# Performance work log

Hardware: AMD Instinct MI355X
Metric: run time of the kernel (lower is better)

The kernel has to match this reference:

```python
import jax, jax.numpy as jnp
import numpy as np

BN_EPS = 1e-5
NORM_EPS = 1e-6


def setup_inputs() -> dict:
    key = jax.random.key(0)
    k1, k2, k3, k4 = jax.random.split(key, 4)
    n_total, d = 200000, 128
    n, s = 50000, 25
    features = jax.random.normal(k1, (n_total, d), dtype=jnp.float32)
    self_idx = jax.random.randint(k2, (n,), 0, n_total, dtype=jnp.int64)
    neigh_idx = jax.random.randint(k3, (n, s), 0, n_total, dtype=jnp.int64)
    W = jax.random.normal(k4, (d, 2 * d), dtype=jnp.float32) / jnp.sqrt(2.0 * d)
    b = jnp.zeros((d,), dtype=jnp.float32)
    gamma = jnp.ones((d,), dtype=jnp.float32)
    beta = jnp.zeros((d,), dtype=jnp.float32)
    return {"features": features, "self_idx": self_idx, "neigh_idx": neigh_idx,
            "W": W, "b": b, "gamma": gamma, "beta": beta}


def reference(features, self_idx, neigh_idx, W, b, gamma, beta):
    # mean-aggregate sampled neighbor features: [N, S, D] -> [N, D]
    agg = jnp.mean(features[neigh_idx], axis=1)
    # concat self features with aggregated neighbor features: [N, 2D]
    h = jnp.concatenate([features[self_idx], agg], axis=1)
    # linear -> relu
    out = jax.nn.relu(h @ W.T + b)
    # batchnorm (training mode: batch statistics, biased variance)
    mu = jnp.mean(out, axis=0)
    var = jnp.var(out, axis=0)
    out = (out - mu) * jax.lax.rsqrt(var + BN_EPS) * gamma + beta
    # (dropout p=0 -> identity)
    # row-wise L2 normalize
    norm = jnp.linalg.norm(out, axis=1, keepdims=True)
    return out / (norm + NORM_EPS)
```

## Files before the change

kernel.cpp:

```cpp
#include <hip/hip_runtime.h>
#include <math.h>

typedef __attribute__((ext_vector_type(8))) short short8;
typedef __attribute__((ext_vector_type(4))) float f32x4;
typedef unsigned short ushort_t;
typedef unsigned int uint_t;

#define D 128
#define TWO_D 256
#define S_NEIGH 25

static constexpr float BN_EPS_C = 1e-5f;
static constexpr float NORM_EPS_C = 1e-6f;

__device__ __forceinline__ uint_t f2bf_bits(float f) {
    uint_t u = __float_as_uint(f);
    return (u + 0x7FFFu + ((u >> 16) & 1u)) >> 16;
}

__device__ __forceinline__ void conv8(const float* __restrict__ src, ushort_t* __restrict__ dst) {
    const float4 f0 = *(const float4*)(src);
    const float4 f1 = *(const float4*)(src + 4);
    uint_t o[4];
    o[0] = f2bf_bits(f0.x) | (f2bf_bits(f0.y) << 16);
    o[1] = f2bf_bits(f0.z) | (f2bf_bits(f0.w) << 16);
    o[2] = f2bf_bits(f1.x) | (f2bf_bits(f1.y) << 16);
    o[3] = f2bf_bits(f1.z) | (f2bf_bits(f1.w) << 16);
    *(uint4*)(dst) = *(uint4*)o;
}

__global__ __launch_bounds__(256) void k_conv(const float* __restrict__ feat,
                                              ushort_t* __restrict__ feat16,
                                              const float* __restrict__ W,
                                              ushort_t* __restrict__ Wb,
                                              float* __restrict__ stats) {
    const long i0 = ((long)blockIdx.x * 256 + threadIdx.x) * 8;
    conv8(feat + i0, feat16 + i0);
    if (blockIdx.x < 16) {
        conv8(W + i0, Wb + i0);
    }
    if (blockIdx.x == 16 && threadIdx.x < 256) stats[threadIdx.x] = 0.0f;
}

__global__ __launch_bounds__(256, 3) void k_gather16(
    const ushort_t* __restrict__ feat16,
    const int* __restrict__ self_idx,
    const int* __restrict__ neigh_idx,
    ushort_t* __restrict__ h16, int N)
{
    __shared__ int s_nidx[64 * S_NEIGH];
    __shared__ int s_sidx[64];
    const int t = threadIdx.x;
    const int base = blockIdx.x * 64;
    const int nvalid = min(64, N - base);
    const int V = nvalid * S_NEIGH;
    const long goff = (long)base * S_NEIGH;
    for (int i = t; i < (64 * S_NEIGH) / 4; i += 256) {
        const int e0 = 4 * i;
        if (e0 + 3 < V) {
            ((int4*)s_nidx)[i] = *(const int4*)(neigh_idx + goff + e0);
        } else {
            #pragma unroll
            for (int e = 0; e < 4; ++e)
                if (e0 + e < V) s_nidx[e0 + e] = neigh_idx[goff + e0 + e];
        }
    }
    if (t < 64 && t < nvalid) s_sidx[t] = self_idx[base + t];
    __syncthreads();

    const int g = t >> 4;
    const int l16 = t & 15;
    const int eoff = l16 * 8;
    #pragma unroll
    for (int rep = 0; rep < 4; ++rep) {
        const int n = rep * 16 + g;
        if (n < nvalid) {
            const long gn = base + n;
            const uint4 sf = *(const uint4*)(feat16 + (long)s_sidx[n] * D + eoff);
            *(uint4*)(h16 + gn * TWO_D + eoff) = sf;
            const int* nid = s_nidx + n * S_NEIGH;
            float ae[8] = {0.f,0.f,0.f,0.f,0.f,0.f,0.f,0.f};
            float ao[8] = {0.f,0.f,0.f,0.f,0.f,0.f,0.f,0.f};
            #pragma unroll
            for (int b = 0; b < 2; ++b) {
                uint4 buf[12];
                #pragma unroll
                for (int u = 0; u < 12; ++u)
                    buf[u] = *(const uint4*)(feat16 + (long)nid[b * 12 + u] * D + eoff);
                #pragma unroll
                for (int u = 0; u < 12; ++u) {
                    const uint_t* pu = (const uint_t*)&buf[u];
                    float* ac = (u & 1) ? ao : ae;
                    #pragma unroll
                    for (int j = 0; j < 4; ++j) {
                        const uint_t w = pu[j];
                        ac[2 * j]     += __uint_as_float(w << 16);
                        ac[2 * j + 1] += __uint_as_float(w & 0xFFFF0000u);
                    }
                }
            }
            {
                const uint4 f24 = *(const uint4*)(feat16 + (long)nid[24] * D + eoff);
                const uint_t* pu = (const uint_t*)&f24;
                #pragma unroll
                for (int j = 0; j < 4; ++j) {
                    const uint_t w = pu[j];
                    ae[2 * j]     += __uint_as_float(w << 16);
                    ae[2 * j + 1] += __uint_as_float(w & 0xFFFF0000u);
                }
            }
            const float r = 1.0f / S_NEIGH;
            uint_t o[4];
            #pragma unroll
            for (int j = 0; j < 4; ++j)
                o[j] = f2bf_bits((ae[2 * j] + ao[2 * j]) * r) |
                       (f2bf_bits((ae[2 * j + 1] + ao[2 * j + 1]) * r) << 16);
            *(uint4*)(h16 + gn * TWO_D + D + eoff) = *(uint4*)o;
        }
    }
}

__global__ __launch_bounds__(256, 4) void k_gather32(
    const float* __restrict__ feat,
    const int* __restrict__ self_idx,
    const int* __restrict__ neigh_idx,
    ushort_t* __restrict__ h16, int N)
{
    __shared__ int s_nidx[64 * S_NEIGH];
    __shared__ int s_sidx[64];
    const int t = threadIdx.x;
    const int base = blockIdx.x * 64;
    const int nvalid = min(64, N - base);
    const int V = nvalid * S_NEIGH;
    const long goff = (long)base * S_NEIGH;
    for (int i = t; i < (64 * S_NEIGH) / 4; i += 256) {
        const int e0 = 4 * i;
        if (e0 + 3 < V) {
            ((int4*)s_nidx)[i] = *(const int4*)(neigh_idx + goff + e0);
        } else {
            #pragma unroll
            for (int e = 0; e < 4; ++e)
                if (e0 + e < V) s_nidx[e0 + e] = neigh_idx[goff + e0 + e];
        }
    }
    if (t < 64 && t < nvalid) s_sidx[t] = self_idx[base + t];
    __syncthreads();

    const int g = t >> 5;
    const int l32 = t & 31;
    const int eoff = l32 * 4;
    #pragma unroll
    for (int rep = 0; rep < 8; ++rep) {
        const int n = rep * 8 + g;
        if (n < nvalid) {
            const long gn = base + n;
            const float4 sf = *(const float4*)(feat + (long)s_sidx[n] * D + eoff);
            uint_t so[2];
            so[0] = f2bf_bits(sf.x) | (f2bf_bits(sf.y) << 16);
            so[1] = f2bf_bits(sf.z) | (f2bf_bits(sf.w) << 16);
            *(uint2*)(h16 + gn * TWO_D + eoff) = *(uint2*)so;
            const int* nid = s_nidx + n * S_NEIGH;
            float a0 = 0.f, a1 = 0.f, a2 = 0.f, a3 = 0.f;
            #pragma unroll
            for (int b = 0; b < 5; ++b) {
                float4 buf[5];
                #pragma unroll
                for (int u = 0; u < 5; ++u)
                    buf[u] = *(const float4*)(feat + (long)nid[b * 5 + u] * D + eoff);
                #pragma unroll
                for (int u = 0; u < 5; ++u) {
                    a0 += buf[u].x; a1 += buf[u].y; a2 += buf[u].z; a3 += buf[u].w;
                }
            }
            const float r = 1.0f / S_NEIGH;
            uint_t o[2];
            o[0] = f2bf_bits(a0 * r) | (f2bf_bits(a1 * r) << 16);
            o[1] = f2bf_bits(a2 * r) | (f2bf_bits(a3 * r) << 16);
            *(uint2*)(h16 + gn * TWO_D + D + eoff) = *(uint2*)o;
        }
    }
}

__global__ __launch_bounds__(512, 2) void k_gemm(
    const ushort_t* __restrict__ h16,
    const ushort_t* __restrict__ Wb,
    const float* __restrict__ bias,
    ushort_t* __restrict__ out1b,
    float* __restrict__ stats,
    int N)
{
    __shared__ ushort_t lds_b[32768];
    __shared__ float lds_s[8][D];
    __shared__ float lds_q[8][D];

    const int t = threadIdx.x;
    #pragma unroll
    for (int it = 0; it < 8; ++it) {
        const int i = it * 512 + t;
        const int row = i >> 5;
        const int gr  = i & 31;
        const uint4 v = *(const uint4*)(Wb + row * TWO_D + gr * 8);
        *(uint4*)(lds_b + row * TWO_D + ((gr ^ (row & 7)) * 8)) = v;
    }
    __syncthreads();

    const int wv = t >> 6;
    const int l  = t & 63;
    const int lm = l & 15;
    const int lh = l >> 4;
    const int mb = blockIdx.x * 128 + wv * 16;

    short8 a[8];
    const long arow = (long)(mb + lm) * TWO_D;
    #pragma unroll
    for (int ks = 0; ks < 8; ++ks)
        a[ks] = *(const short8*)(h16 + arow + ks * 32 + lh * 8);

    f32x4 acc[8];
    #pragma unroll
    for (int nt = 0; nt < 8; ++nt) {
        const float bc = bias[nt * 16 + lm];
        acc[nt] = (f32x4){bc, bc, bc, bc};
    }

    #pragma unroll
    for (int nt = 0; nt < 8; ++nt) {
        const int colrow = nt * 16 + lm;
        #pragma unroll
        for (int ks = 0; ks < 8; ++ks) {
            const short8 b = *(const short8*)(lds_b + colrow * TWO_D +
                                              (((ks * 4 + lh) ^ (l & 7)) * 8));
            acc[nt] = __builtin_amdgcn_mfma_f32_16x16x32_bf16(a[ks], b, acc[nt], 0, 0, 0);
        }
    }

    #pragma unroll
    for (int nt = 0; nt < 8; ++nt) {
        float cs = 0.f, cq = 0.f;
        #pragma unroll
        for (int r = 0; r < 4; ++r) {
            const int node = mb + lh * 4 + r;
            const float v = fmaxf(acc[nt][r], 0.f);
            if (node < N) {
                out1b[(long)node * D + nt * 16 + lm] = (ushort_t)f2bf_bits(v);
                cs += v; cq += v * v;
            }
        }
        cs += __shfl_xor(cs, 16); cq += __shfl_xor(cq, 16);
        cs += __shfl_xor(cs, 32); cq += __shfl_xor(cq, 32);
        if (l < 16) { lds_s[wv][nt * 16 + l] = cs; lds_q[wv][nt * 16 + l] = cq; }
    }
    __syncthreads();
    if (t < D) {
        float s = 0.f;
        #pragma unroll
        for (int w = 0; w < 8; ++w) s += lds_s[w][t];
        atomicAdd(&stats[t], s);
    } else if (t < TWO_D) {
        const int j = t - D;
        float q = 0.f;
        #pragma unroll
        for (int w = 0; w < 8; ++w) q += lds_q[w][j];
        atomicAdd(&stats[D + j], q);
    }
}

__global__ __launch_bounds__(256) void k_final(
    const ushort_t* __restrict__ out1b,
    float* __restrict__ out,
    const float* __restrict__ stats,
    const float* __restrict__ gamma,
    const float* __restrict__ beta,
    int N)
{
    __shared__ float scale[D];
    __shared__ float shift[D];
    const int t = threadIdx.x;
    if (t < D) {
        const float invN = 1.0f / (float)N;
        const float mu = stats[t] * invN;
        const float var = stats[D + t] * invN - mu * mu;
        const float sc = gamma[t] * rsqrtf(var + BN_EPS_C);
        scale[t] = sc;
        shift[t] = beta[t] - mu * sc;
    }
    __syncthreads();

    const int row = blockIdx.x * 8 + (t >> 5);
    const int l = t & 31;
    if (row < N) {
        const uint2 xb = *(const uint2*)(out1b + (long)row * D + 4 * l);
        float x0 = __uint_as_float(xb.x << 16);
        float x1 = __uint_as_float(xb.x & 0xFFFF0000u);
        float x2 = __uint_as_float(xb.y << 16);
        float x3 = __uint_as_float(xb.y & 0xFFFF0000u);
        const float4 s4 = *(const float4*)&scale[4 * l];
        const float4 f4 = *(const float4*)&shift[4 * l];
        float4 y;
        y.x = x0 * s4.x + f4.x;
        y.y = x1 * s4.y + f4.y;
        y.z = x2 * s4.z + f4.z;
        y.w = x3 * s4.w + f4.w;
        float ss = y.x*y.x + y.y*y.y + y.z*y.z + y.w*y.w;
        #pragma unroll
        for (int m = 16; m >= 1; m >>= 1) ss += __shfl_xor(ss, m);
        const float inv = 1.0f / (sqrtf(ss) + NORM_EPS_C);
        y.x *= inv; y.y *= inv; y.z *= inv; y.w *= inv;
        *(float4*)(out + (long)row * D + 4 * l) = y;
    }
}

extern "C" void kernel_launch(void* const* d_in, const int* in_sizes, int n_in,
                              void* d_out, int out_size, void* d_ws, size_t ws_size,
                              hipStream_t stream) {
    const float* feat      = (const float*)d_in[0];
    const int*   self_idx  = (const int*)d_in[1];
    const int*   neigh_idx = (const int*)d_in[2];
    const float* W         = (const float*)d_in[3];
    const float* b         = (const float*)d_in[4];
    const float* gamma     = (const float*)d_in[5];
    const float* beta      = (const float*)d_in[6];
    float* out = (float*)d_out;
    const int N = in_sizes[1];
    const long n_total = in_sizes[0] / D;
    const int gblk = (N + 63) / 64;
    const int mblk = (N + 127) / 128;
    const long nr = (long)mblk * 128;

    const size_t feat16_bytes = (size_t)n_total * D * 2;
    const size_t h16_bytes    = (size_t)nr * TWO_D * 2;
    const size_t o1_bytes     = (size_t)nr * D * 2;
    const size_t wb_bytes     = (size_t)D * TWO_D * 2;
    const size_t stats_bytes  = 256 * 4;
    const bool full = ws_size >= feat16_bytes + h16_bytes + o1_bytes + wb_bytes + stats_bytes;

    char* p = (char*)d_ws;
    ushort_t* feat16 = nullptr;
    if (full) { feat16 = (ushort_t*)p; p += feat16_bytes; }
    ushort_t* h16   = (ushort_t*)p; p += h16_bytes;
    ushort_t* out1b = (ushort_t*)p; p += o1_bytes;
    ushort_t* Wb    = (ushort_t*)p; p += wb_bytes;
    float* stats    = (float*)p;

    if (full) {
        k_conv<<<(int)(n_total * D / (256 * 8)), 256, 0, stream>>>(feat, feat16, W, Wb, stats);
        k_gather16<<<gblk, 256, 0, stream>>>(feat16, self_idx, neigh_idx, h16, N);
    } else {
        k_conv<<<16, 256, 0, stream>>>(W, Wb, W, Wb, stats);
        hipMemsetAsync(stats, 0, 256 * 4, stream);
        k_gather32<<<gblk, 256, 0, stream>>>(feat, self_idx, neigh_idx, h16, N);
    }
    k_gemm<<<mblk, 512, 0, stream>>>(h16, Wb, b, out1b, stats, N);
    k_final<<<(N + 7) / 8, 256, 0, stream>>>(out1b, out, stats, gamma, beta, N);
}
```

Measured before the change: 104.0 us.

## Fuse GEMM, batchnorm and L2 normalize via cooperative grid sync

Adds a cooperative-launch kernel that runs the GEMM with ReLU, accumulates batch statistics with atomics, and then waits on a grid-wide barrier. After the barrier it applies batchnorm and row L2 normalization directly from the register accumulators. This removes the bf16 intermediate output write and read-back and the separate final kernel launch. The cost is a grid sync, a launch that requires every block to be resident at once, and per-call host queries of device attributes and occupancy. The old two-kernel path remains as a fallback when cooperative launch is unavailable.

```diff
diff --git a/kernel.cpp b/kernel.cpp
--- a/kernel.cpp
+++ b/kernel.cpp
@@ -1,5 +1,8 @@
 #include <hip/hip_runtime.h>
+#include <hip/hip_cooperative_groups.h>
 #include <math.h>
+
+namespace cg = cooperative_groups;
 
 typedef __attribute__((ext_vector_type(8))) short short8;
 typedef __attribute__((ext_vector_type(4))) float f32x4;
@@ -181,6 +184,131 @@
     }
 }
 
+__global__ __launch_bounds__(512, 4) void k_gemm_fused(
+    const ushort_t* __restrict__ h16,
+    const ushort_t* __restrict__ Wb,
+    const float* __restrict__ bias,
+    const float* __restrict__ gamma,
+    const float* __restrict__ beta,
+    float* __restrict__ out,
+    float* __restrict__ stats,
+    int N)
+{
+    __shared__ ushort_t lds_b[32768];
+    __shared__ float lds_s[8][D];
+    __shared__ float lds_q[8][D];
+
+    const int t = threadIdx.x;
+    #pragma unroll
+    for (int it = 0; it < 8; ++it) {
+        const int i = it * 512 + t;
+        const int row = i >> 5;
+        const int gr  = i & 31;
+        const uint4 v = *(const uint4*)(Wb + row * TWO_D + gr * 8);
+        *(uint4*)(lds_b + row * TWO_D + ((gr ^ (row & 7)) * 8)) = v;
+    }
+    __syncthreads();
+
+    const int wv = t >> 6;
+    const int l  = t & 63;
+    const int lm = l & 15;
+    const int lh = l >> 4;
+    const int mb = blockIdx.x * 128 + wv * 16;
+
+    short8 a[8];
+    const long arow = (long)(mb + lm) * TWO_D;
+    #pragma unroll
+    for (int ks = 0; ks < 8; ++ks)
+        a[ks] = *(const short8*)(h16 + arow + ks * 32 + lh * 8);
+
+    f32x4 acc[8];
+    #pragma unroll
+    for (int nt = 0; nt < 8; ++nt) {
+        const float bc = bias[nt * 16 + lm];
+        acc[nt] = (f32x4){bc, bc, bc, bc};
+    }
+
+    #pragma unroll
+    for (int nt = 0; nt < 8; ++nt) {
+        const int colrow = nt * 16 + lm;
+        #pragma unroll
+        for (int ks = 0; ks < 8; ++ks) {
+            const short8 b = *(const short8*)(lds_b + colrow * TWO_D +
+                                              (((ks * 4 + lh) ^ (l & 7)) * 8));
+            acc[nt] = __builtin_amdgcn_mfma_f32_16x16x32_bf16(a[ks], b, acc[nt], 0, 0, 0);
+        }
+    }
+
+    #pragma unroll
+    for (int nt = 0; nt < 8; ++nt) {
+        float cs = 0.f, cq = 0.f;
+        #pragma unroll
+        for (int r = 0; r < 4; ++r) {
+            const float v = fmaxf(acc[nt][r], 0.f);
+            acc[nt][r] = v;
+            if (mb + lh * 4 + r < N) { cs += v; cq += v * v; }
+        }
+        cs += __shfl_xor(cs, 16); cq += __shfl_xor(cq, 16);
+        cs += __shfl_xor(cs, 32); cq += __shfl_xor(cq, 32);
+        if (l < 16) { lds_s[wv][nt * 16 + l] = cs; lds_q[wv][nt * 16 + l] = cq; }
+    }
+    __syncthreads();
+    if (t < D) {
+        float s = 0.f;
+        #pragma unroll
+        for (int w = 0; w < 8; ++w) s += lds_s[w][t];
+        atomicAdd(&stats[t], s);
+    } else if (t < TWO_D) {
+        const int j = t - D;
+        float q = 0.f;
+        #pragma unroll
+        for (int w = 0; w < 8; ++w) q += lds_q[w][j];
+        atomicAdd(&stats[D + j], q);
+    }
+
+    cg::this_grid().sync();
+
+    float* scale = &lds_s[0][0];
+    float* shift = &lds_q[0][0];
+    if (t < D) {
+        const float invN = 1.0f / (float)N;
+        const float mu = stats[t] * invN;
+        const float var = stats[D + t] * invN - mu * mu;
+        const float sc = gamma[t] * rsqrtf(var + BN_EPS_C);
+        scale[t] = sc;
+        shift[t] = beta[t] - mu * sc;
+    }
+    __syncthreads();
+
+    float sc8[8], sh8[8];
+    #pragma unroll
+    for (int nt = 0; nt < 8; ++nt) {
+        sc8[nt] = scale[nt * 16 + lm];
+        sh8[nt] = shift[nt * 16 + lm];
+    }
+
+    #pragma unroll
+    for (int r = 0; r < 4; ++r) {
+        float ss = 0.f;
+        #pragma unroll
+        for (int nt = 0; nt < 8; ++nt) {
+            const float y = acc[nt][r] * sc8[nt] + sh8[nt];
+            ss += y * y;
+        }
+        ss += __shfl_xor(ss, 1); ss += __shfl_xor(ss, 2);
+        ss += __shfl_xor(ss, 4); ss += __shfl_xor(ss, 8);
+        const float inv = 1.0f / (sqrtf(ss) + NORM_EPS_C);
+        const int node = mb + lh * 4 + r;
+        if (node < N) {
+            #pragma unroll
+            for (int nt = 0; nt < 8; ++nt) {
+                const float y = acc[nt][r] * sc8[nt] + sh8[nt];
+                out[(long)node * D + nt * 16 + lm] = y * inv;
+            }
+        }
+    }
+}
+
 __global__ __launch_bounds__(512, 2) void k_gemm(
     const ushort_t* __restrict__ h16,
     const ushort_t* __restrict__ Wb,
@@ -350,6 +478,22 @@
         hipMemsetAsync(stats, 0, 256 * 4, stream);
         k_gather32<<<gblk, 256, 0, stream>>>(feat, self_idx, neigh_idx, h16, N);
     }
-    k_gemm<<<mblk, 512, 0, stream>>>(h16, Wb, b, out1b, stats, N);
-    k_final<<<(N + 7) / 8, 256, 0, stream>>>(out1b, out, stats, gamma, beta, N);
-}
+
+    int dev = 0;
+    hipGetDevice(&dev);
+    int coopAttr = 0, nCU = 0, maxB = 0;
+    hipDeviceGetAttribute(&coopAttr, hipDeviceAttributeCooperativeLaunch, dev);
+    hipDeviceGetAttribute(&nCU, hipDeviceAttributeMultiprocessorCount, dev);
+    hipOccupancyMaxActiveBlocksPerMultiprocessor(&maxB, k_gemm_fused, 512, 0);
+    const bool coop = coopAttr && ((long)maxB * nCU >= mblk);
+
+    if (coop) {
+        void* args[] = {(void*)&h16, (void*)&Wb, (void*)&b, (void*)&gamma,
+                        (void*)&beta, (void*)&out, (void*)&stats, (void*)&N};
+        hipLaunchCooperativeKernel((void*)k_gemm_fused, dim3(mblk), dim3(512),
+                                   args, 0, stream);
+    } else {
+        k_gemm<<<mblk, 512, 0, stream>>>(h16, Wb, b, out1b, stats, N);
+        k_final<<<(N + 7) / 8, 256, 0, stream>>>(out1b, out, stats, gamma, beta, N);
+    }
+}
```

New measurement: 103.8 us. No clear change (-0.2%).

## Fuse neighbor gather-mean with linear layer GEMM through LDS

Applied to the files above, without the earlier changes.

The bf16 gather/mean kernel and the GEMM kernel become one kernel per 64-node block. The concatenated self/aggregated rows are built in swizzled shared memory instead of being written to and reread from a global h16 buffer. Each block then runs MFMA against register-held weight slices and accumulates the batchnorm statistics with atomics. This removes the h16 global round trip and one launch, at the cost of 32 KB+ LDS per block and 64-row tiles that reload W per block.

```diff
diff --git a/kernel.cpp b/kernel.cpp
--- a/kernel.cpp
+++ b/kernel.cpp
@@ -42,81 +42,148 @@
     if (blockIdx.x == 16 && threadIdx.x < 256) stats[threadIdx.x] = 0.0f;
 }
 
-__global__ __launch_bounds__(256, 3) void k_gather16(
+__global__ __launch_bounds__(512, 4) void k_fused(
     const ushort_t* __restrict__ feat16,
     const int* __restrict__ self_idx,
     const int* __restrict__ neigh_idx,
-    ushort_t* __restrict__ h16, int N)
+    const ushort_t* __restrict__ Wb,
+    const float* __restrict__ bias,
+    ushort_t* __restrict__ out1b,
+    float* __restrict__ stats,
+    int N)
 {
     __shared__ int s_nidx[64 * S_NEIGH];
     __shared__ int s_sidx[64];
+    __shared__ ushort_t h_lds[64 * TWO_D];
+
     const int t = threadIdx.x;
     const int base = blockIdx.x * 64;
     const int nvalid = min(64, N - base);
-    const int V = nvalid * S_NEIGH;
-    const long goff = (long)base * S_NEIGH;
-    for (int i = t; i < (64 * S_NEIGH) / 4; i += 256) {
-        const int e0 = 4 * i;
-        if (e0 + 3 < V) {
-            ((int4*)s_nidx)[i] = *(const int4*)(neigh_idx + goff + e0);
-        } else {
-            #pragma unroll
-            for (int e = 0; e < 4; ++e)
-                if (e0 + e < V) s_nidx[e0 + e] = neigh_idx[goff + e0 + e];
-        }
-    }
-    if (t < 64 && t < nvalid) s_sidx[t] = self_idx[base + t];
-    __syncthreads();
-
-    const int g = t >> 4;
-    const int l16 = t & 15;
-    const int eoff = l16 * 8;
-    #pragma unroll
-    for (int rep = 0; rep < 4; ++rep) {
-        const int n = rep * 16 + g;
-        if (n < nvalid) {
-            const long gn = base + n;
-            const uint4 sf = *(const uint4*)(feat16 + (long)s_sidx[n] * D + eoff);
-            *(uint4*)(h16 + gn * TWO_D + eoff) = sf;
-            const int* nid = s_nidx + n * S_NEIGH;
-            float ae[8] = {0.f,0.f,0.f,0.f,0.f,0.f,0.f,0.f};
-            float ao[8] = {0.f,0.f,0.f,0.f,0.f,0.f,0.f,0.f};
-            #pragma unroll
-            for (int b = 0; b < 2; ++b) {
-                uint4 buf[12];
+
+    {
+        const int V = nvalid * S_NEIGH;
+        const long goff = (long)base * S_NEIGH;
+        if (t < (64 * S_NEIGH) / 4) {
+            const int e0 = 4 * t;
+            if (e0 + 3 < V) {
+                ((int4*)s_nidx)[t] = *(const int4*)(neigh_idx + goff + e0);
+            } else {
                 #pragma unroll
-                for (int u = 0; u < 12; ++u)
-                    buf[u] = *(const uint4*)(feat16 + (long)nid[b * 12 + u] * D + eoff);
+                for (int e = 0; e < 4; ++e)
+                    if (e0 + e < V) s_nidx[e0 + e] = neigh_idx[goff + e0 + e];
+            }
+        } else if (t >= 448) {
+            const int i = t - 448;
+            if (i < nvalid) s_sidx[i] = self_idx[base + i];
+        }
+    }
+    __syncthreads();
+
+    {
+        const int g = t >> 4;
+        const int l16 = t & 15;
+        const int eoff = l16 * 8;
+        #pragma unroll
+        for (int rep = 0; rep < 2; ++rep) {
+            const int n = rep * 32 + g;
+            ushort_t* hrow = h_lds + n * TWO_D;
+            const int gs = (l16 ^ (n & 7)) * 8;
+            const int ga = ((16 + l16) ^ (n & 7)) * 8;
+            if (n < nvalid) {
+                const uint4 sf = *(const uint4*)(feat16 + (long)s_sidx[n] * D + eoff);
+                *(uint4*)(hrow + gs) = sf;
+                const int* nid = s_nidx + n * S_NEIGH;
+                float ae[8] = {0.f,0.f,0.f,0.f,0.f,0.f,0.f,0.f};
+                float ao[8] = {0.f,0.f,0.f,0.f,0.f,0.f,0.f,0.f};
                 #pragma unroll
-                for (int u = 0; u < 12; ++u) {
-                    const uint_t* pu = (const uint_t*)&buf[u];
-                    float* ac = (u & 1) ? ao : ae;
+                for (int b = 0; b < 2; ++b) {
+                    uint4 buf[12];
+                    #pragma unroll
+                    for (int u = 0; u < 12; ++u)
+                        buf[u] = *(const uint4*)(feat16 + (long)nid[b * 12 + u] * D + eoff);
+                    #pragma unroll
+                    for (int u = 0; u < 12; ++u) {
+                        const uint_t* pu = (const uint_t*)&buf[u];
+                        float* ac = (u & 1) ? ao : ae;
+                        #pragma unroll
+                        for (int j = 0; j < 4; ++j) {
+                            const uint_t w = pu[j];
+                            ac[2 * j]     += __uint_as_float(w << 16);
+                            ac[2 * j + 1] += __uint_as_float(w & 0xFFFF0000u);
+                        }
+                    }
+                }
+                {
+                    const uint4 f24 = *(const uint4*)(feat16 + (long)nid[24] * D + eoff);
+                    const uint_t* pu = (const uint_t*)&f24;
                     #pragma unroll
                     for (int j = 0; j < 4; ++j) {
                         const uint_t w = pu[j];
-                        ac[2 * j]     += __uint_as_float(w << 16);
-                        ac[2 * j + 1] += __uint_as_float(w & 0xFFFF0000u);
+                        ae[2 * j]     += __uint_as_float(w << 16);
+                        ae[2 * j + 1] += __uint_as_float(w & 0xFFFF0000u);
                     }
                 }
+                const float r = 1.0f / S_NEIGH;
+                uint_t o[4];
+                #pragma unroll
+                for (int j = 0; j < 4; ++j)
+                    o[j] = f2bf_bits((ae[2 * j] + ao[2 * j]) * r) |
+                           (f2bf_bits((ae[2 * j + 1] + ao[2 * j + 1]) * r) << 16);
+                *(uint4*)(hrow + ga) = *(uint4*)o;
+            } else {
+                const uint4 z = make_uint4(0, 0, 0, 0);
+                *(uint4*)(hrow + gs) = z;
+                *(uint4*)(hrow + ga) = z;
             }
-            {
-                const uint4 f24 = *(const uint4*)(feat16 + (long)nid[24] * D + eoff);
-                const uint_t* pu = (const uint_t*)&f24;
-                #pragma unroll
-                for (int j = 0; j < 4; ++j) {
-                    const uint_t w = pu[j];
-                    ae[2 * j]     += __uint_as_float(w << 16);
-                    ae[2 * j + 1] += __uint_as_float(w & 0xFFFF0000u);
-                }
+        }
+    }
+    __syncthreads();
+
+    const int wv = t >> 6;
+    const int l  = t & 63;
+    const int lm = l & 15;
+    const int lh = l >> 4;
+    const int colg = 16 * wv + lm;
+
+    short8 b_reg[8];
+    #pragma unroll
+    for (int ks = 0; ks < 8; ++ks)
+        b_reg[ks] = *(const short8*)(Wb + (long)colg * TWO_D + ks * 32 + lh * 8);
+
+    const float bc = bias[colg];
+    f32x4 acc[4];
+    #pragma unroll
+    for (int mt = 0; mt < 4; ++mt) acc[mt] = (f32x4){bc, bc, bc, bc};
+
+    #pragma unroll
+    for (int mt = 0; mt < 4; ++mt) {
+        const int arow = mt * 16 + lm;
+        #pragma unroll
+        for (int ks = 0; ks < 8; ++ks) {
+            const short8 a = *(const short8*)(h_lds + arow * TWO_D +
+                                              (((ks * 4 + lh) ^ (lm & 7)) * 8));
+            acc[mt] = __builtin_amdgcn_mfma_f32_16x16x32_bf16(a, b_reg[ks], acc[mt], 0, 0, 0);
+        }
+    }
+
+    float cs = 0.f, cq = 0.f;
+    #pragma unroll
+    for (int mt = 0; mt < 4; ++mt) {
+        #pragma unroll
+        for (int r = 0; r < 4; ++r) {
+            const int node = base + mt * 16 + lh * 4 + r;
+            const float v = fmaxf(acc[mt][r], 0.f);
+            if (node < N) {
+                out1b[(long)node * D + colg] = (ushort_t)f2bf_bits(v);
+                cs += v; cq += v * v;
             }
-            const float r = 1.0f / S_NEIGH;
-            uint_t o[4];
-            #pragma unroll
-            for (int j = 0; j < 4; ++j)
-                o[j] = f2bf_bits((ae[2 * j] + ao[2 * j]) * r) |
-                       (f2bf_bits((ae[2 * j + 1] + ao[2 * j + 1]) * r) << 16);
-            *(uint4*)(h16 + gn * TWO_D + D + eoff) = *(uint4*)o;
-        }
+        }
+    }
+    cs += __shfl_xor(cs, 16); cq += __shfl_xor(cq, 16);
+    cs += __shfl_xor(cs, 32); cq += __shfl_xor(cq, 32);
+    if (l < 16) {
+        atomicAdd(&stats[16 * wv + l], cs);
+        atomicAdd(&stats[D + 16 * wv + l], cq);
     }
 }
 
@@ -344,12 +411,12 @@
 
     if (full) {
         k_conv<<<(int)(n_total * D / (256 * 8)), 256, 0, stream>>>(feat, feat16, W, Wb, stats);
-        k_gather16<<<gblk, 256, 0, stream>>>(feat16, self_idx, neigh_idx, h16, N);
+        k_fused<<<gblk, 512, 0, stream>>>(feat16, self_idx, neigh_idx, Wb, b, out1b, stats, N);
     } else {
         k_conv<<<16, 256, 0, stream>>>(W, Wb, W, Wb, stats);
         hipMemsetAsync(stats, 0, 256 * 4, stream);
         k_gather32<<<gblk, 256, 0, stream>>>(feat, self_idx, neigh_idx, h16, N);
-    }
-    k_gemm<<<mblk, 512, 0, stream>>>(h16, Wb, b, out1b, stats, N);
+        k_gemm<<<mblk, 512, 0, stream>>>(h16, Wb, b, out1b, stats, N);
+    }
     k_final<<<(N + 7) / 8, 256, 0, stream>>>(out1b, out, stats, gamma, beta, N);
 }
```

Measured after the change: 95.70 us. 8.0% less time.
